# Kernel optimization log

Hardware: AMD Instinct MI355X
Metric: run time of the kernel (lower is better)

Reference implementation:

```python
import jax, jax.numpy as jnp
import numpy as np

B, N1, N2, D, K, KC = 2, 4096, 4096, 64, 16, 8
MLP = [128, 128, 128]
HID = [8, 8]


def _knn_idx(q, db, k):
    # q:[B,S,C] db:[B,M,C] -> indices of k smallest squared distances [B,S,k]
    d = (jnp.sum(q * q, -1)[..., None]
         - 2.0 * jnp.einsum('bsc,bmc->bsm', q, db)
         + jnp.sum(db * db, -1)[:, None, :])
    d = jnp.maximum(d, 0.0)
    _, idx = jax.lax.top_k(-d, k)
    return idx


def _group(points, idx):
    # points:[B,M,C], idx:[B,S,K] -> [B,S,K,C]
    return jax.vmap(lambda p, i: p[i])(points, idx)


def _conv_chain(x, params, act):
    # 1x1 Conv2d chain on x:[B,C,K,N]
    for w, b in params:
        x = act(jnp.einsum('oi,bikn->bokn', w, x) + b[None, :, None, None])
    return x


def setup_inputs():
    key = jax.random.key(0)
    ks = jax.random.split(key, 40)

    def p(i, shape, s=0.05):
        return jax.random.normal(ks[i], shape, jnp.float32) * s

    inp = {
        'xyz1': p(0, (B, 3, N1), 1.0), 'xyz2': p(1, (B, 3, N2), 1.0),
        'points1': p(2, (B, D, N1), 1.0), 'points2': p(3, (B, D, N2), 1.0),
        'vel1': p(4, (B, N1), 1.0), 'vel2': p(5, (B, N2), 1.0),
        'mask1': jnp.ones((B, N1), bool), 'mask2': jnp.ones((B, N2), bool),
        'final_cluster_coords': p(6, (B, N1, KC, 3), 1.0),
        'final_cluster_vel': p(7, (B, N1, KC), 1.0),
        'w_xyz': jnp.asarray(0.4, jnp.float32),
        'w_vel': jnp.asarray(0.2, jnp.float32),
        'w_points': jnp.asarray(0.4, jnp.float32),
    }
    dims = [2 * D + 3] + MLP
    for i in range(3):
        inp[f'mlp_w{i}'] = p(8 + i, (dims[i + 1], dims[i]))
        inp[f'mlp_b{i}'] = p(11 + i, (dims[i + 1],))
    wdims = [3] + HID + [MLP[-1]]
    for i in range(3):
        inp[f'wn1_w{i}'] = p(14 + i, (wdims[i + 1], wdims[i]), 0.5)
        inp[f'wn1_b{i}'] = p(17 + i, (wdims[i + 1],), 0.5)
        inp[f'wn2_w{i}'] = p(20 + i, (wdims[i + 1], wdims[i]), 0.5)
        inp[f'wn2_b{i}'] = p(23 + i, (wdims[i + 1],), 0.5)
    return inp


def reference(xyz1, xyz2, points1, points2, vel1, vel2, mask1, mask2,
              final_cluster_coords, final_cluster_vel,
              w_xyz, w_vel, w_points,
              mlp_w0, mlp_b0, mlp_w1, mlp_b1, mlp_w2, mlp_b2,
              wn1_w0, wn1_b0, wn1_w1, wn1_b1, wn1_w2, wn1_b2,
              wn2_w0, wn2_b0, wn2_w1, wn2_b1, wn2_w2, wn2_b2):
    leaky = lambda x: jnp.where(x >= 0, x, 0.1 * x)  # LeakyReLU(0.1)
    relu = jax.nn.relu
    x1 = xyz1.transpose(0, 2, 1)   # [B,N1,3]
    x2 = xyz2.transpose(0, 2, 1)   # [B,N2,3]
    p1 = points1.transpose(0, 2, 1)  # [B,N1,D]
    p2 = points2.transpose(0, 2, 1)  # [B,N2,D]

    u = final_cluster_coords / jnp.linalg.norm(final_cluster_coords, axis=-1, keepdims=True)
    ATA = jnp.einsum('bnki,bnkj->bnij', u, u) + 1e-6 * jnp.eye(3, dtype=u.dtype)
    ATb = jnp.einsum('bnki,bnk->bni', u, final_cluster_vel)
    v_world = jnp.linalg.solve(ATA, ATb[..., None])[..., 0]  # [B,N1,3]
    u1 = x1 / jnp.linalg.norm(x1, axis=-1, keepdims=True)
    err = jnp.abs(jnp.sum(v_world * u1, -1) - vel1)
    mask = err <= 5.0  # [B,N1]

    # --- cross-frame KNN in weighted feature space ---
    f1 = jnp.concatenate([w_xyz * x1, w_points * p1], -1)
    f2 = jnp.concatenate([w_xyz * x2, w_points * p2], -1)
    idx = _knn_idx(f1, f2, K)                       # [B,N1,K]
    dxyz = _group(x2, idx) - x1[:, :, None, :]      # [B,N1,K,3]
    gp2 = _group(p2, idx)                           # [B,N1,K,D]
    gp1 = jnp.broadcast_to(p1[:, :, None, :], gp2.shape)
    new_pts = jnp.concatenate([gp1, gp2, dxyz], -1).transpose(0, 3, 2, 1)  # [B,2D+3,K,N1]
    new_pts = _conv_chain(new_pts, [(mlp_w0, mlp_b0), (mlp_w1, mlp_b1), (mlp_w2, mlp_b2)], leaky)
    w1 = _conv_chain(dxyz.transpose(0, 3, 2, 1),
                     [(wn1_w0, wn1_b0), (wn1_w1, wn1_b1), (wn1_w2, wn1_b2)], relu)
    p2p = jnp.sum(w1 * new_pts, axis=2)  # [B,Cout,N1]

    # --- patch-to-patch aggregation with rigidity-weighted features ---
    mf = mask[..., None].astype(x1.dtype)
    w_r = mf * 0.9 + (1.0 - mf) * 0.1
    w_f = mf * 0.1 + (1.0 - mf) * 0.9
    comb = jnp.concatenate([w_f * f1, w_r * v_world], -1)
    idx2 = _knn_idx(comb, comb, K)
    dxyz2 = _group(x1, idx2) - x1[:, :, None, :]
    w2 = _conv_chain(dxyz2.transpose(0, 3, 2, 1),
                     [(wn2_w0, wn2_b0), (wn2_w1, wn2_b1), (wn2_w2, wn2_b2)], relu)
    gcost = _group(p2p.transpose(0, 2, 1), idx2)     # [B,N1,K,Cout]
    patch = jnp.sum(w2 * gcost.transpose(0, 3, 2, 1), axis=2)  # [B,Cout,N1]
    return patch, v_world
```

## Files before the change

kernel.cpp:

```cpp
#include <hip/hip_runtime.h>
#include <hip/hip_bf16.h>

typedef __hip_bfloat16 bf16;
typedef unsigned long long u64;
typedef __bf16 bf16x8 __attribute__((ext_vector_type(8)));
typedef __bf16 bf16x4 __attribute__((ext_vector_type(4)));
typedef _Float16 f16x8 __attribute__((ext_vector_type(8)));
typedef _Float16 f16x4 __attribute__((ext_vector_type(4)));
typedef float  f32x4  __attribute__((ext_vector_type(4)));

#define Bsz 2
#define Np  4096
#define Dch 64
#define Kn  16
#define KCn 8
#define DIMA 67
#define DIMB 70
#define CH  128
#define POSB 64
#define XS   168
#define TS   104
#define MS   24
#define MR   10
#define WNSZ 1256
#define PHALF (Bsz*Np*2*MS)


#define OFF_P1T  0
#define OFF_P2T  (Bsz*Np*Dch)
#define OFF_P2P  (2*Bsz*Np*Dch)
#define OFF_IDX1 (OFF_P2P + Bsz*Np*CH)
#define OFF_IDX2 (OFF_IDX1 + Bsz*Np*Kn)
#define OFF_F1N  (OFF_IDX2 + Bsz*Np*Kn)
#define OFF_F2N  (OFF_F1N + Bsz*Np)
#define OFF_CBN  (OFF_F2N + Bsz*Np)
#define OFF_WF   (OFF_CBN + Bsz*Np)
#define OFF_WR   (OFF_WF + Bsz*Np)
#define OFF_VW   (OFF_WR + Bsz*Np)
#define OFF_BF   (OFF_VW + 3*Bsz*Np)
#define BFSZ     (Bsz*Np*TS)
#define OFF_WPK  (OFF_BF + 3*BFSZ)

__device__ __forceinline__ int sniff_bf(const void* wxyz) {
    float v = __bfloat162float(((const bf16*)wxyz)[0]);
    return (fabsf(v - 0.4f) < 0.05f) ? 1 : 0;
}
__device__ __forceinline__ float ldin(const void* p, long i, int isbf) {
    return isbf ? __bfloat162float(((const bf16*)p)[i]) : ((const float*)p)[i];
}
__device__ __forceinline__ void stout(void* p, long i, float v, int isbf) {
    if (isbf) ((bf16*)p)[i] = __float2bfloat16(v);
    else      ((float*)p)[i] = v;
}
__device__ __forceinline__ u64 shfl_xor_u64(u64 v, int m) {
    int lo = __shfl_xor((int)(unsigned)(v & 0xFFFFFFFFu), m, 64);
    int hi = __shfl_xor((int)(unsigned)(v >> 32), m, 64);
    return ((u64)(unsigned)hi << 32) | (unsigned)lo;
}
__device__ __forceinline__ void hlsplit(float x, _Float16* hp, _Float16* lp) {
    _Float16 h = (_Float16)x;
    *hp = h;
    *lp = (_Float16)(x - (float)h);
}
__device__ __forceinline__ void gload_lds16(const void* g, void* l) {
    __builtin_amdgcn_global_load_lds(
        (const __attribute__((address_space(1))) unsigned int*)g,
        (__attribute__((address_space(3))) unsigned int*)l,
        16, 0, 0);
}

__global__ __launch_bounds__(256) void pack_kernel(
    const void* __restrict__ wxyz,
    const void* __restrict__ mw0, const void* __restrict__ mb0,
    const void* __restrict__ mw1, const void* __restrict__ mb1,
    const void* __restrict__ mw2, const void* __restrict__ mb2,
    const void* __restrict__ n1w0, const void* __restrict__ n1b0,
    const void* __restrict__ n1w1, const void* __restrict__ n1b1,
    const void* __restrict__ n1w2, const void* __restrict__ n1b2,
    const void* __restrict__ n2w0, const void* __restrict__ n2b0,
    const void* __restrict__ n2w1, const void* __restrict__ n2b1,
    const void* __restrict__ n2w2, const void* __restrict__ n2b2,
    __bf16* __restrict__ Wp, float* __restrict__ bp,
    float* __restrict__ wn1p, float* __restrict__ wn2p)
{
    int isbf = sniff_bf(wxyz);
    int t0 = blockIdx.x * 256 + threadIdx.x;
    int NT = gridDim.x * 256;
    for (int i = t0; i < 3*CH*XS; i += NT) {
        int L = i / (CH*XS), r = i - L*(CH*XS);
        int o = r / XS, c = r - o*XS;
        int dimIn = (L == 0) ? 131 : 128;
        const void* Wg = (L == 0) ? mw0 : ((L == 1) ? mw1 : mw2);
        Wp[i] = (c < dimIn) ? (__bf16)ldin(Wg, (long)o*dimIn + c, isbf) : (__bf16)0.f;
    }
    for (int i = t0; i < 3*CH; i += NT) {
        int L = i >> 7, o = i & 127;
        const void* Bg = (L == 0) ? mb0 : ((L == 1) ? mb1 : mb2);
        bp[i] = ldin(Bg, o, isbf);
    }
    for (int i = t0; i < WNSZ; i += NT) {
        float v1, v2;
        if (i < 1024)      { v1 = ldin(n1w2, i, isbf);        v2 = ldin(n2w2, i, isbf); }
        else if (i < 1152) { v1 = ldin(n1b2, i-1024, isbf);   v2 = ldin(n2b2, i-1024, isbf); }
        else if (i < 1176) { v1 = ldin(n1w0, i-1152, isbf);   v2 = ldin(n2w0, i-1152, isbf); }
        else if (i < 1184) { v1 = ldin(n1b0, i-1176, isbf);   v2 = ldin(n2b0, i-1176, isbf); }
        else if (i < 1248) { v1 = ldin(n1w1, i-1184, isbf);   v2 = ldin(n2w1, i-1184, isbf); }
        else               { v1 = ldin(n1b1, i-1248, isbf);   v2 = ldin(n2b1, i-1248, isbf); }
        wn1p[i] = v1; wn2p[i] = v2;
    }
}

__global__ __launch_bounds__(64) void prep_pt_kernel(
    const void* __restrict__ xyz1, const void* __restrict__ vel1,
    const void* __restrict__ fcc, const void* __restrict__ fcv,
    const void* __restrict__ wxyz, const void* __restrict__ xyz2,
    _Float16* __restrict__ f1hi, _Float16* __restrict__ f1lo,
    _Float16* __restrict__ cbhi, _Float16* __restrict__ cblo,
    float* __restrict__ f1n, float* __restrict__ cbn,
    float* __restrict__ wfA, float* __restrict__ wrA, float* __restrict__ vwA,
    void* __restrict__ outv,
    _Float16* __restrict__ f2hi, float* __restrict__ f2n)
{
    int isbf = sniff_bf(wxyz);
    float wx = ldin(wxyz, 0, isbf);
    if (blockIdx.x >= (Bsz*Np)/64) {
        int gid = (blockIdx.x - (Bsz*Np)/64) * 64 + threadIdx.x;
        int b = gid >> 12, n = gid & (Np - 1);
        _Float16* fh = f2hi + (size_t)gid * TS;
        float nn = 0.f;
        #pragma unroll
        for (int j = 0; j < 3; j++) {
            float v = wx * ldin(xyz2, (b*3+j)*Np + n, isbf);
            nn += v*v;
            fh[64+j] = (_Float16)v;
        }
        f2n[gid] = nn;
        return;
    }
    int gid = blockIdx.x * 64 + threadIdx.x;
    int b = gid >> 12, n = gid & (Np - 1);

    float a00=0.f,a01=0.f,a02=0.f,a11=0.f,a12=0.f,a22=0.f,r0=0.f,r1=0.f,r2=0.f;
    for (int k = 0; k < KCn; k++) {
        long base = ((long)gid * KCn + k) * 3;
        float x = ldin(fcc, base, isbf), y = ldin(fcc, base+1, isbf), z = ldin(fcc, base+2, isbf);
        float inv = 1.0f / sqrtf(x*x + y*y + z*z);
        float ux = x*inv, uy = y*inv, uz = z*inv;
        a00 += ux*ux; a01 += ux*uy; a02 += ux*uz;
        a11 += uy*uy; a12 += uy*uz; a22 += uz*uz;
        float v = ldin(fcv, (long)gid * KCn + k, isbf);
        r0 += ux*v; r1 += uy*v; r2 += uz*v;
    }
    a00 += 1e-6f; a11 += 1e-6f; a22 += 1e-6f;
    float c00 = a11*a22 - a12*a12;
    float c01 = a02*a12 - a01*a22;
    float c02 = a01*a12 - a02*a11;
    float det = a00*c00 + a01*c01 + a02*c02;
    float id  = 1.0f / det;
    float c11 = a00*a22 - a02*a02;
    float c12 = a01*a02 - a00*a12;
    float c22 = a00*a11 - a01*a01;
    float vx = (c00*r0 + c01*r1 + c02*r2) * id;
    float vy = (c01*r0 + c11*r1 + c12*r2) * id;
    float vz = (c02*r0 + c12*r1 + c22*r2) * id;

    stout(outv, (long)Bsz*CH*Np + gid*3 + 0, vx, isbf);
    stout(outv, (long)Bsz*CH*Np + gid*3 + 1, vy, isbf);
    stout(outv, (long)Bsz*CH*Np + gid*3 + 2, vz, isbf);
    vwA[gid*3+0] = vx; vwA[gid*3+1] = vy; vwA[gid*3+2] = vz;

    float x0 = ldin(xyz1, (b*3+0)*Np + n, isbf);
    float x1 = ldin(xyz1, (b*3+1)*Np + n, isbf);
    float x2 = ldin(xyz1, (b*3+2)*Np + n, isbf);
    float invn = 1.0f / sqrtf(x0*x0 + x1*x1 + x2*x2);
    float dotv = vx*(x0*invn) + vy*(x1*invn) + vz*(x2*invn);
    float err = fabsf(dotv - ldin(vel1, gid, isbf));
    bool msk = (err <= 5.0f);
    float w_f = msk ? 0.1f : 0.9f;
    float w_r = msk ? 0.9f : 0.1f;
    wfA[gid] = w_f; wrA[gid] = w_r;

    _Float16* fh = f1hi + (size_t)gid * TS;
    _Float16* fl = f1lo + (size_t)gid * TS;
    _Float16* ch = cbhi + (size_t)gid * TS;
    _Float16* cl = cblo + (size_t)gid * TS;
    float nn = 0.f, cn = 0.f;
    float xs[3] = {x0, x1, x2};
    #pragma unroll
    for (int j = 0; j < 3; j++) {
        float v = wx * xs[j]; nn += v*v; hlsplit(v, fh+64+j, fl+64+j);
        float c = w_f * v;    cn += c*c; hlsplit(c, ch+64+j, cl+64+j);
    }
    float vv[3] = {vx, vy, vz};
    #pragma unroll
    for (int j = 0; j < 3; j++) {
        float c = w_r * vv[j]; cn += c*c; hlsplit(c, ch+67+j, cl+67+j);
    }
    f1n[gid] = nn;
    cbn[gid] = cn;
}

__global__ __launch_bounds__(256) void prep_ch_kernel(
    const void* __restrict__ points1, const void* __restrict__ points2,
    const void* __restrict__ wxyz, const void* __restrict__ wpts,
    const float* __restrict__ wfA,
    _Float16* __restrict__ f1hi, _Float16* __restrict__ f1lo,
    _Float16* __restrict__ cbhi, _Float16* __restrict__ cblo,
    float* __restrict__ p1t, float* __restrict__ f1n, float* __restrict__ cbn,
    _Float16* __restrict__ f2hi,
    float* __restrict__ p2t, float* __restrict__ f2n)
{
    __shared__ float tile[16 * 64];
    int t = threadIdx.x;
    int isbf = sniff_bf(wxyz);
    float wp = ldin(wpts, 0, isbf);
    int fr = blockIdx.x >> 9;
    int g0 = (blockIdx.x & 511) * 16;
    int b = g0 >> 12;
    const void* pts = fr ? points2 : points1;
    _Float16* fhi = fr ? f2hi : f1hi;
    float* ptt = fr ? p2t : p1t;
    float* fn  = fr ? f2n : f1n;
    int do_cb = !fr;

    {
        int n16 = t & 15, cc = t >> 4;
        int n = (g0 + n16) & (Np - 1);
        #pragma unroll
        for (int it = 0; it < 4; it++) {
            int c = cc + it * 16;
            tile[n16 * 64 + c] = ldin(pts, (long)(b * Dch + c) * Np + n, isbf);
        }
    }
    __syncthreads();

    int p = t >> 4, j = t & 15;
    int gid = g0 + p;
    float wf = do_cb ? wfA[gid] : 0.f;
    float nn = 0.f, cn = 0.f;
    f16x4 h4, l4, ch4, cl4;
    float pv4[4];
    #pragma unroll
    for (int i = 0; i < 4; i++) {
        float pv = tile[p * 64 + 4 * j + i];
        pv4[i] = pv;
        float v = wp * pv; nn += v * v;
        _Float16 hh, ll; hlsplit(v, &hh, &ll);
        h4[i] = hh; l4[i] = ll;
        float c = wf * v; cn += c * c;
        _Float16 chh, cll; hlsplit(c, &chh, &cll);
        ch4[i] = chh; cl4[i] = cll;
    }
    *(f16x4*)(fhi + (size_t)gid * TS + 4 * j) = h4;
    if (do_cb) {
        *(f16x4*)(f1lo + (size_t)gid * TS + 4 * j) = l4;
        *(f16x4*)(cbhi + (size_t)gid * TS + 4 * j) = ch4;
        *(f16x4*)(cblo + (size_t)gid * TS + 4 * j) = cl4;
    }
    float4 pq = { pv4[0], pv4[1], pv4[2], pv4[3] };
    *(float4*)(ptt + (size_t)gid * Dch + 4 * j) = pq;

    #pragma unroll
    for (int s = 1; s < 16; s <<= 1) {
        nn += __shfl_xor(nn, s, 64);
        cn += __shfl_xor(cn, s, 64);
    }
    if (j == 0) {
        fn[gid] += nn;
        if (do_cb) cbn[gid] += cn;
    }
}

__global__ __launch_bounds__(256, 8) void knn_kernel(
    const _Float16* __restrict__ f1hi, const _Float16* __restrict__ f1lo,
    const float* __restrict__ f1n,
    const _Float16* __restrict__ f2hi, const float* __restrict__ f2n,
    const _Float16* __restrict__ cbhi, const _Float16* __restrict__ cblo,
    const float* __restrict__ cbn,
    unsigned* __restrict__ part)
{
    __shared__ __align__(16) _Float16 Th[64 * TS];
    __shared__ unsigned dkey[64 * 17 + 16];

    int t = threadIdx.x;
    int prob = blockIdx.x >> 10;
    int bid = blockIdx.x & 1023;
    int qblk = bid >> 1, half = bid & 1;
    int qbase = qblk * 16;
    int b = qbase >> 12;

    const _Float16* qhi = prob ? cbhi : f1hi;
    const _Float16* qlo = prob ? cblo : f1lo;
    const float*  qn  = prob ? cbn  : f1n;
    const _Float16* dbh = (prob ? cbhi : f2hi) + (size_t)b * Np * TS;
    const float*  dnb = (prob ? cbn  : f2n) + (size_t)b * Np;
    unsigned* pout = part + (size_t)prob * PHALF;

    int qi = t >> 4, w = t & 15;
    int wv = t >> 6, lane = t & 63, quad = lane >> 4, col = lane & 15;

    f16x8 qfh[3], qfl[3];
    #pragma unroll
    for (int kb = 0; kb < 3; kb++) {
        qfh[kb] = *(const f16x8*)(qhi + (size_t)(qbase + col) * TS + kb*32 + quad*8);
        qfl[kb] = *(const f16x8*)(qlo + (size_t)(qbase + col) * TS + kb*32 + quad*8);
    }
    float qn4[4];
    #pragma unroll
    for (int r = 0; r < 4; r++) qn4[r] = qn[qbase + quad*4 + r];

    unsigned bd[MR];
    #pragma unroll
    for (int i = 0; i < MR; i++) bd[i] = 0xFFFFFFFFu;

    for (int T = 0; T < Np / 128; T++) {
        int Tg = half * (Np / 128) + T;
        {
            const float4* sh = (const float4*)(dbh + (size_t)Tg * 64 * TS);
            float4* dh = (float4*)Th;
            for (int i = t; i < 64 * 13; i += 256)
                gload_lds16(sh + i, dh + i);
        }
        __syncthreads();

        f32x4 acc = {0.f, 0.f, 0.f, 0.f};
        #pragma unroll
        for (int kb = 0; kb < 3; kb++) {
            f16x8 bh = *(const f16x8*)(Th + (wv*16 + col) * TS + kb*32 + quad*8);
            acc = __builtin_amdgcn_mfma_f32_16x16x32_f16(qfh[kb], bh, acc, 0, 0, 0);
            acc = __builtin_amdgcn_mfma_f32_16x16x32_f16(qfl[kb], bh, acc, 0, 0, 0);
        }
        float tn = dnb[Tg * 64 + wv*16 + col];
        unsigned lidx = (unsigned)(T*64 + wv*16 + col);
        #pragma unroll
        for (int r = 0; r < 4; r++) {
            int m = quad*4 + r;
            float d = fmaxf(qn4[r] - 2.f * acc[r] + tn, 0.f);
            dkey[(wv*16 + col) * 17 + m] = (__float_as_uint(d) & 0xFFFFF800u) | lidx;
        }
        __syncthreads();

        #pragma unroll
        for (int p = 0; p < 4; p++) {
            unsigned key = dkey[(w + p*16) * 17 + qi];
            if (key < bd[MR-1]) {
                bd[MR-1] = key;
                #pragma unroll
                for (int j = MR-2; j >= 0; j--) {
                    unsigned lo = bd[j] < bd[j+1] ? bd[j] : bd[j+1];
                    unsigned hi = bd[j] < bd[j+1] ? bd[j+1] : bd[j];
                    bd[j] = lo; bd[j+1] = hi;
                }
            }
        }
    }

    unsigned win1 = 0, win2 = 0;
    #pragma unroll
    for (int o = 0; o < MS; o++) {
        unsigned v = bd[0];
        #pragma unroll
        for (int s = 1; s < 16; s <<= 1) {
            unsigned u = (unsigned)__shfl_xor((int)v, s, 64);
            v = u < v ? u : v;
        }
        if (w == o) win1 = v;
        if (w == o - 16) win2 = v;
        if (bd[0] == v) {
            #pragma unroll
            for (int j = 0; j < MR-1; j++) bd[j] = bd[j+1];
            bd[MR-1] = 0xFFFFFFFFu;
        }
    }
    size_t base = ((size_t)(qbase + qi) * 2 + half) * MS;
    pout[base + w] = (win1 & 0x7FFu) + (unsigned)half * 2048u;
    if (w < MS - 16) pout[base + 16 + w] = (win2 & 0x7FFu) + (unsigned)half * 2048u;
}

__global__ __launch_bounds__(256) void knn_rescue_kernel(
    const unsigned* __restrict__ part,
    const void* __restrict__ xyz1, const void* __restrict__ xyz2,
    const float* __restrict__ p1t, const float* __restrict__ p2t,
    const float* __restrict__ f1n, const float* __restrict__ f2n,
    const float* __restrict__ cbn,
    const float* __restrict__ wfA, const float* __restrict__ wrA,
    const float* __restrict__ vwA,
    const void* __restrict__ wxyz, const void* __restrict__ wpts,
    int* __restrict__ idx1, int* __restrict__ idx2)
{
    __shared__ float qrow[4][64];
    __shared__ float qmisc[4][12];

    int t = threadIdx.x, wv = t >> 6, l = t & 63;
    int isbf = sniff_bf(wxyz);
    float wx = ldin(wxyz, 0, isbf), wp = ldin(wpts, 0, isbf);
    int mode = blockIdx.x >> 11;
    int qb = blockIdx.x & 2047;
    int q = qb * 4 + wv;
    int b = q >> 12, n = q & (Np - 1);

    const void* xyzc = mode ? xyz1 : xyz2;
    const float* ptc = mode ? p1t : p2t;
    const float* qnA = mode ? cbn : f1n;
    const float* cnA = mode ? cbn : f2n;
    const unsigned* pp = part + (size_t)mode * PHALF;
    int* out = mode ? idx2 : idx1;

    if (l < 16) ((float4*)qrow[wv])[l] = *(const float4*)(p1t + (size_t)q * Dch + l*4);
    if (l == 16) {
        qmisc[wv][0] = ldin(xyz1, (b*3+0)*Np + n, isbf);
        qmisc[wv][1] = ldin(xyz1, (b*3+1)*Np + n, isbf);
        qmisc[wv][2] = ldin(xyz1, (b*3+2)*Np + n, isbf);
        qmisc[wv][3] = qnA[q];
        if (mode == 1) {
            qmisc[wv][4] = wfA[q]; qmisc[wv][5] = wrA[q];
            qmisc[wv][6] = vwA[q*3+0]; qmisc[wv][7] = vwA[q*3+1]; qmisc[wv][8] = vwA[q*3+2];
        }
    }
    __syncthreads();

    u64 key = 0xFFFFFFFFFFFFFFFFULL;
    if (l < 2 * MS) {
        unsigned pk = pp[(size_t)q * (2*MS) + l];
        int m = (int)pk & (Np - 1);
        const float* crow = ptc + (size_t)(b * Np + m) * Dch;
        float sp = 0.f;
        #pragma unroll
        for (int i = 0; i < 16; i++) {
            float4 qv = ((const float4*)qrow[wv])[i];
            float4 cv = *(const float4*)(crow + i*4);
            sp = fmaf(qv.x, cv.x, sp); sp = fmaf(qv.y, cv.y, sp);
            sp = fmaf(qv.z, cv.z, sp); sp = fmaf(qv.w, cv.w, sp);
        }
        float sx = 0.f;
        #pragma unroll
        for (int j = 0; j < 3; j++)
            sx = fmaf(qmisc[wv][j], ldin(xyzc, (b*3+j)*Np + m, isbf), sx);
        float dot;
        if (mode == 0) {
            dot = wx*wx*sx + wp*wp*sp;
        } else {
            float sv = qmisc[wv][6]*vwA[(size_t)(b*Np+m)*3+0]
                     + qmisc[wv][7]*vwA[(size_t)(b*Np+m)*3+1]
                     + qmisc[wv][8]*vwA[(size_t)(b*Np+m)*3+2];
            dot = qmisc[wv][4]*wfA[b*Np+m]*(wx*wx*sx + wp*wp*sp)
                + qmisc[wv][5]*wrA[b*Np+m]*sv;
        }
        float d = fmaxf(qmisc[wv][3] - 2.f*dot + cnA[b*Np + m], 0.f);
        key = ((u64)__float_as_uint(d) << 32) | (unsigned)m;
    }

    #pragma unroll
    for (int k = 2; k <= 64; k <<= 1) {
        #pragma unroll
        for (int j = k >> 1; j >= 1; j >>= 1) {
            u64 p = shfl_xor_u64(key, j);
            bool up   = ((l & k) == 0);
            bool lowh = ((l & j) == 0);
            u64 mn = (key < p) ? key : p;
            u64 mx = (key < p) ? p : key;
            key = (up == lowh) ? mn : mx;
        }
    }
    if (l < Kn) out[(size_t)q * Kn + l] = (int)(key & 0xFFFFFFFFu);
}

__global__ __launch_bounds__(256) void mlp_mfma_kernel(
    const void* __restrict__ xyz1, const void* __restrict__ xyz2,
    const float* __restrict__ p1t, const float* __restrict__ p2t,
    const int* __restrict__ idx1, const void* __restrict__ wxyz,
    const __bf16* __restrict__ Wp, const float* __restrict__ bp,
    const float* __restrict__ wn1p,
    float* __restrict__ p2p)
{
    __shared__ __align__(16) __bf16 X[POSB * XS];
    __shared__ __align__(16) __bf16 Wt[CH * XS];
    __shared__ float biasS[CH];
    __shared__ float dxs[POSB * 4];
    __shared__ float h2s[POSB * 8];
    __shared__ float wnS[WNSZ];
    __shared__ int   nidx[POSB];

    int t = threadIdx.x;
    int isbf = sniff_bf(wxyz);
    int ng0 = blockIdx.x * 4;
    int bidx = ng0 >> 12;

    for (int i = t; i < WNSZ; i += 256) wnS[i] = wn1p[i];
    if (t < POSB) {
        int nl = t >> 4, k = t & 15;
        nidx[t] = idx1[(size_t)(ng0 + nl) * Kn + k] & (Np - 1);
    }
    __syncthreads();

    for (int i = t; i < POSB * 32; i += 256) {
        int pos = i >> 5, g = i & 31;
        int nl = pos >> 4, ng = ng0 + nl, m = nidx[pos];
        float4 v = (g < 16) ? ((const float4*)(p1t + (size_t)ng * Dch))[g]
                            : ((const float4*)(p2t + (size_t)(bidx*Np + m) * Dch))[g - 16];
        bf16x4 o4 = { (__bf16)v.x, (__bf16)v.y, (__bf16)v.z, (__bf16)v.w };
        *(bf16x4*)(X + pos * XS + g * 4) = o4;
    }
    if (t < POSB) {
        int nl = t >> 4, ng = ng0 + nl, m = nidx[t];
        #pragma unroll
        for (int j = 0; j < 3; j++) {
            float dv = ldin(xyz2, (bidx*3+j)*Np + m, isbf)
                     - ldin(xyz1, (bidx*3+j)*Np + (ng & (Np-1)), isbf);
            X[t*XS + 128 + j] = (__bf16)dv;
            dxs[t*4 + j] = dv;
        }
        for (int c = 131; c < XS; c++) X[t*XS + c] = (__bf16)0.f;
    }

    int wv = t >> 6, lane = t & 63, quad = lane >> 4, col = lane & 15;

    #pragma unroll
    for (int L = 0; L < 3; L++) {
        const int KK = (L == 0) ? 160 : 128;
        __syncthreads();
        {
            const float4* src = (const float4*)(Wp + (size_t)L * CH * XS);
            for (int i = t; i < CH * XS / 8; i += 256) ((float4*)Wt)[i] = src[i];
        }
        if (t < CH) biasS[t] = bp[L * CH + t];
        __syncthreads();

        f32x4 acc[8];
        #pragma unroll
        for (int nt = 0; nt < 8; nt++) {
            float bv = biasS[nt * 16 + col];
            f32x4 a; a[0] = bv; a[1] = bv; a[2] = bv; a[3] = bv;
            acc[nt] = a;
        }
        for (int kb = 0; kb < KK / 32; kb++) {
            bf16x8 af = *(const bf16x8*)(X + (16*wv + col) * XS + kb*32 + quad*8);
            #pragma unroll
            for (int nt = 0; nt < 8; nt++) {
                bf16x8 bfr = *(const bf16x8*)(Wt + (nt*16 + col) * XS + kb*32 + quad*8);
                acc[nt] = __builtin_amdgcn_mfma_f32_16x16x32_bf16(af, bfr, acc[nt], 0, 0, 0);
            }
        }
        #pragma unroll
        for (int nt = 0; nt < 8; nt++) {
            #pragma unroll
            for (int r = 0; r < 4; r++) {
                float v = acc[nt][r];
                v = (v >= 0.f) ? v : 0.1f * v;
                X[(16*wv + quad*4 + r) * XS + nt*16 + col] = (__bf16)v;
            }
        }
    }
    __syncthreads();

    const float* wn_w2 = wnS;
    const float* wn_b2 = wnS + 1024;
    const float* wn_w0 = wnS + 1152;
    const float* wn_b0 = wnS + 1176;
    const float* wn_w1 = wnS + 1184;
    const float* wn_b1 = wnS + 1248;

    if (t < POSB) {
        float h1[8];
        #pragma unroll
        for (int j = 0; j < 8; j++) {
            float s = wn_b0[j];
            #pragma unroll
            for (int i = 0; i < 3; i++) s += wn_w0[j*3+i] * dxs[t*4+i];
            h1[j] = fmaxf(s, 0.f);
        }
        #pragma unroll
        for (int j = 0; j < 8; j++) {
            float s = wn_b1[j];
            #pragma unroll
            for (int i = 0; i < 8; i++) s += wn_w1[j*8+i] * h1[i];
            h2s[t*8+j] = fmaxf(s, 0.f);
        }
    }
    __syncthreads();

    for (int o = t; o < 4 * CH; o += 256) {
        int nl = o >> 7, c = o & 127;
        float acc = 0.f;
        for (int k = 0; k < Kn; k++) {
            int pos = nl*16 + k;
            float s = wn_b2[c];
            #pragma unroll
            for (int j = 0; j < 8; j++) s += wn_w2[c*8+j] * h2s[pos*8+j];
            s = fmaxf(s, 0.f);
            acc += s * (float)X[pos * XS + c];
        }
        p2p[(size_t)(ng0 + nl) * CH + c] = acc;
    }
}

__global__ __launch_bounds__(256) void patch_kernel(
    const void* __restrict__ xyz1, const float* __restrict__ p2p,
    const int* __restrict__ idx2, const void* __restrict__ wxyz,
    const float* __restrict__ wn2p,
    void* __restrict__ outp)
{
    __shared__ float wnS[WNSZ];
    __shared__ float h2s[128 * 8];
    __shared__ int   nid[128];
    __shared__ float outS[8][132];

    int t = threadIdx.x;
    int bn0 = blockIdx.x * 8;
    int isbf = sniff_bf(wxyz);
    int b = bn0 >> 12, n0 = bn0 & (Np - 1);

    for (int i = t; i < WNSZ; i += 256) wnS[i] = wn2p[i];
    if (t < 128) nid[t] = idx2[(size_t)bn0 * Kn + t] & (Np - 1);
    __syncthreads();

    const float* w2s = wnS;
    const float* b2s = wnS + 1024;
    const float* w0s = wnS + 1152;
    const float* b0s = wnS + 1176;
    const float* w1s = wnS + 1184;
    const float* b1s = wnS + 1248;

    if (t < 128) {
        int q = t >> 4;
        int n = n0 + q;
        int m = nid[t];
        float dx[3];
        #pragma unroll
        for (int j = 0; j < 3; j++)
            dx[j] = ldin(xyz1, (b*3+j)*Np + m, isbf) - ldin(xyz1, (b*3+j)*Np + n, isbf);
        float h1[8];
        #pragma unroll
        for (int j = 0; j < 8; j++) {
            float s = b0s[j];
            #pragma unroll
            for (int i = 0; i < 3; i++) s += w0s[j*3+i] * dx[i];
            h1[j] = fmaxf(s, 0.f);
        }
        #pragma unroll
        for (int j = 0; j < 8; j++) {
            float s = b1s[j];
            #pragma unroll
            for (int i = 0; i < 8; i++) s += w1s[j*8+i] * h1[i];
            h2s[t*8+j] = fmaxf(s, 0.f);
        }
    }
    __syncthreads();

    {
        int c = t & 127, qh = t >> 7;
        #pragma unroll
        for (int qq = 0; qq < 4; qq++) {
            int q = qh + qq*2;
            float acc = 0.f;
            for (int k = 0; k < Kn; k++) {
                int mm = nid[q*16 + k];
                float s = b2s[c];
                #pragma unroll
                for (int j = 0; j < 8; j++) s += w2s[c*8+j] * h2s[(q*16+k)*8+j];
                s = fmaxf(s, 0.f);
                acc += s * p2p[(size_t)(b * Np + mm) * CH + c];
            }
            outS[q][c] = acc;
        }
    }
    __syncthreads();

    if (t < 128) {
        int c = t;
        size_t obase = (size_t)(b*CH + c) * Np + n0;
        if (isbf) {
            bf16x8 o;
            #pragma unroll
            for (int i = 0; i < 8; i++) o[i] = (__bf16)outS[i][c];
            *(bf16x8*)((__bf16*)outp + obase) = o;
        } else {
            float4 o1 = { outS[0][c], outS[1][c], outS[2][c], outS[3][c] };
            float4 o2 = { outS[4][c], outS[5][c], outS[6][c], outS[7][c] };
            *(float4*)((float*)outp + obase) = o1;
            *(float4*)((float*)outp + obase + 4) = o2;
        }
    }
}

extern "C" void kernel_launch(void* const* d_in, const int* in_sizes, int n_in,
                              void* d_out, int out_size, void* d_ws, size_t ws_size,
                              hipStream_t stream)
{
    const void* xyz1    = d_in[0];
    const void* xyz2    = d_in[1];
    const void* points1 = d_in[2];
    const void* points2 = d_in[3];
    const void* vel1    = d_in[4];
    const void* fcc     = d_in[8];
    const void* fcv     = d_in[9];
    const void* wxyz    = d_in[10];
    const void* wpts    = d_in[12];
    const void* mw0 = d_in[13]; const void* mb0 = d_in[14];
    const void* mw1 = d_in[15]; const void* mb1 = d_in[16];
    const void* mw2 = d_in[17]; const void* mb2 = d_in[18];
    const void* w1w0 = d_in[19]; const void* w1b0 = d_in[20];
    const void* w2w0 = d_in[21]; const void* w2b0 = d_in[22];
    const void* w1w1 = d_in[23]; const void* w1b1 = d_in[24];
    const void* w2w1 = d_in[25]; const void* w2b1 = d_in[26];
    const void* w1w2 = d_in[27]; const void* w1b2 = d_in[28];
    const void* w2w2 = d_in[29]; const void* w2b2 = d_in[30];

    float* ws = (float*)d_ws;
    float* p1t  = ws + OFF_P1T;
    float* p2t  = ws + OFF_P2T;
    float* p2p  = ws + OFF_P2P;
    int* idx1 = (int*)(ws + OFF_IDX1);
    int* idx2 = (int*)(ws + OFF_IDX2);
    float* f1n = ws + OFF_F1N;
    float* f2n = ws + OFF_F2N;
    float* cbn = ws + OFF_CBN;
    float* wfA = ws + OFF_WF;
    float* wrA = ws + OFF_WR;
    float* vwA = ws + OFF_VW;
    _Float16* f1hi = (_Float16*)(ws + OFF_BF);
    _Float16* f1lo = f1hi + BFSZ;
    _Float16* f2hi = f1lo + BFSZ;
    _Float16* f2lo = f2hi + BFSZ;
    _Float16* cbhi = f2lo + BFSZ;
    _Float16* cblo = cbhi + BFSZ;
    __bf16* Wp  = (__bf16*)(ws + OFF_WPK);
    float*  bp  = ws + OFF_WPK + (3*CH*XS)/2;
    float*  wn1p = bp + 3*CH;
    float*  wn2p = wn1p + WNSZ;
    unsigned* part = (unsigned*)(ws + OFF_P2P);

    hipMemsetAsync(f1hi, 0, (size_t)6 * BFSZ * sizeof(_Float16), stream);

    pack_kernel<<<64, 256, 0, stream>>>(wxyz,
        mw0, mb0, mw1, mb1, mw2, mb2,
        w1w0, w1b0, w1w1, w1b1, w1w2, w1b2,
        w2w0, w2b0, w2w1, w2b1, w2w2, w2b2,
        Wp, bp, wn1p, wn2p);
    prep_pt_kernel<<<2*(Bsz*Np)/64, 64, 0, stream>>>(xyz1, vel1, fcc, fcv, wxyz, xyz2,
        f1hi, f1lo, cbhi, cblo, f1n, cbn, wfA, wrA, vwA, d_out, f2hi, f2n);
    prep_ch_kernel<<<2*(Bsz*Np)/16, 256, 0, stream>>>(points1, points2, wxyz, wpts, wfA,
        f1hi, f1lo, cbhi, cblo, p1t, f1n, cbn, f2hi, p2t, f2n);
    knn_kernel<<<2*(Bsz*Np)/16*2, 256, 0, stream>>>(f1hi, f1lo, f1n, f2hi, f2n,
        cbhi, cblo, cbn, part);
    knn_rescue_kernel<<<2*(Bsz*Np)/4, 256, 0, stream>>>(part, xyz1, xyz2, p1t, p2t,
        f1n, f2n, cbn, wfA, wrA, vwA, wxyz, wpts, idx1, idx2);
    mlp_mfma_kernel<<<(Bsz*Np)/4, 256, 0, stream>>>(xyz1, xyz2, p1t, p2t, idx1, wxyz,
        Wp, bp, wn1p, p2p);
    patch_kernel<<<(Bsz*Np)/8, 256, 0, stream>>>(xyz1, p2p, idx2, wxyz, wn2p, d_out);
}
```

Before: 365.6 us.

## Drop fp16 low-part split in KNN, shrink candidate list, fuse setup kernels

The KNN distance GEMM now uses only the fp16 high part of each feature, which halves the MFMA count and drops the lo-buffer reads and writes. The per-query candidate list shrinks from 10 to 8 entries. The pack and per-point prep kernels are merged into one launch, and the big memset is replaced by zeroing only the padding lanes. Candidate selection becomes less precise, so the rescue pass has to absorb more near-ties, and neighbours could be missed if fp16 error exceeds the margin the rescue covers.

```diff
diff --git a/kernel.cpp b/kernel.cpp
--- a/kernel.cpp
+++ b/kernel.cpp
@@ -21,7 +21,7 @@
 #define XS   168
 #define TS   104
 #define MS   24
-#define MR   10
+#define MR   8
 #define WNSZ 1256
 #define PHALF (Bsz*Np*2*MS)
 
@@ -57,11 +57,6 @@
     int hi = __shfl_xor((int)(unsigned)(v >> 32), m, 64);
     return ((u64)(unsigned)hi << 32) | (unsigned)lo;
 }
-__device__ __forceinline__ void hlsplit(float x, _Float16* hp, _Float16* lp) {
-    _Float16 h = (_Float16)x;
-    *hp = h;
-    *lp = (_Float16)(x - (float)h);
-}
 __device__ __forceinline__ void gload_lds16(const void* g, void* l) {
     __builtin_amdgcn_global_load_lds(
         (const __attribute__((address_space(1))) unsigned int*)g,
@@ -69,8 +64,15 @@
         16, 0, 0);
 }
 
-__global__ __launch_bounds__(256) void pack_kernel(
-    const void* __restrict__ wxyz,
+__global__ __launch_bounds__(256) void setup_kernel(
+    const void* __restrict__ xyz1, const void* __restrict__ vel1,
+    const void* __restrict__ fcc, const void* __restrict__ fcv,
+    const void* __restrict__ wxyz, const void* __restrict__ xyz2,
+    _Float16* __restrict__ f1hi, _Float16* __restrict__ cbhi,
+    float* __restrict__ f1n, float* __restrict__ cbn,
+    float* __restrict__ wfA, float* __restrict__ wrA, float* __restrict__ vwA,
+    void* __restrict__ outv,
+    _Float16* __restrict__ f2hi, float* __restrict__ f2n,
     const void* __restrict__ mw0, const void* __restrict__ mb0,
     const void* __restrict__ mw1, const void* __restrict__ mb1,
     const void* __restrict__ mw2, const void* __restrict__ mb2,
@@ -83,50 +85,46 @@
     __bf16* __restrict__ Wp, float* __restrict__ bp,
     float* __restrict__ wn1p, float* __restrict__ wn2p)
 {
+    int bid = blockIdx.x, t = threadIdx.x;
     int isbf = sniff_bf(wxyz);
-    int t0 = blockIdx.x * 256 + threadIdx.x;
-    int NT = gridDim.x * 256;
-    for (int i = t0; i < 3*CH*XS; i += NT) {
-        int L = i / (CH*XS), r = i - L*(CH*XS);
-        int o = r / XS, c = r - o*XS;
-        int dimIn = (L == 0) ? 131 : 128;
-        const void* Wg = (L == 0) ? mw0 : ((L == 1) ? mw1 : mw2);
-        Wp[i] = (c < dimIn) ? (__bf16)ldin(Wg, (long)o*dimIn + c, isbf) : (__bf16)0.f;
-    }
-    for (int i = t0; i < 3*CH; i += NT) {
-        int L = i >> 7, o = i & 127;
-        const void* Bg = (L == 0) ? mb0 : ((L == 1) ? mb1 : mb2);
-        bp[i] = ldin(Bg, o, isbf);
-    }
-    for (int i = t0; i < WNSZ; i += NT) {
-        float v1, v2;
-        if (i < 1024)      { v1 = ldin(n1w2, i, isbf);        v2 = ldin(n2w2, i, isbf); }
-        else if (i < 1152) { v1 = ldin(n1b2, i-1024, isbf);   v2 = ldin(n2b2, i-1024, isbf); }
-        else if (i < 1176) { v1 = ldin(n1w0, i-1152, isbf);   v2 = ldin(n2w0, i-1152, isbf); }
-        else if (i < 1184) { v1 = ldin(n1b0, i-1176, isbf);   v2 = ldin(n2b0, i-1176, isbf); }
-        else if (i < 1248) { v1 = ldin(n1w1, i-1184, isbf);   v2 = ldin(n2w1, i-1184, isbf); }
-        else               { v1 = ldin(n1b1, i-1248, isbf);   v2 = ldin(n2b1, i-1248, isbf); }
-        wn1p[i] = v1; wn2p[i] = v2;
-    }
-}
-
-__global__ __launch_bounds__(64) void prep_pt_kernel(
-    const void* __restrict__ xyz1, const void* __restrict__ vel1,
-    const void* __restrict__ fcc, const void* __restrict__ fcv,
-    const void* __restrict__ wxyz, const void* __restrict__ xyz2,
-    _Float16* __restrict__ f1hi, _Float16* __restrict__ f1lo,
-    _Float16* __restrict__ cbhi, _Float16* __restrict__ cblo,
-    float* __restrict__ f1n, float* __restrict__ cbn,
-    float* __restrict__ wfA, float* __restrict__ wrA, float* __restrict__ vwA,
-    void* __restrict__ outv,
-    _Float16* __restrict__ f2hi, float* __restrict__ f2n)
-{
-    int isbf = sniff_bf(wxyz);
+    const f16x8 z8 = {0,0,0,0,0,0,0,0};
+
+    if (bid >= 64) {
+        int t0 = (bid - 64) * 256 + t;
+        int NT = 64 * 256;
+        for (int i = t0; i < 3*CH*XS; i += NT) {
+            int L = i / (CH*XS), r = i - L*(CH*XS);
+            int o = r / XS, c = r - o*XS;
+            int dimIn = (L == 0) ? 131 : 128;
+            const void* Wg = (L == 0) ? mw0 : ((L == 1) ? mw1 : mw2);
+            Wp[i] = (c < dimIn) ? (__bf16)ldin(Wg, (long)o*dimIn + c, isbf) : (__bf16)0.f;
+        }
+        for (int i = t0; i < 3*CH; i += NT) {
+            int L = i >> 7, o = i & 127;
+            const void* Bg = (L == 0) ? mb0 : ((L == 1) ? mb1 : mb2);
+            bp[i] = ldin(Bg, o, isbf);
+        }
+        for (int i = t0; i < WNSZ; i += NT) {
+            float v1, v2;
+            if (i < 1024)      { v1 = ldin(n1w2, i, isbf);        v2 = ldin(n2w2, i, isbf); }
+            else if (i < 1152) { v1 = ldin(n1b2, i-1024, isbf);   v2 = ldin(n2b2, i-1024, isbf); }
+            else if (i < 1176) { v1 = ldin(n1w0, i-1152, isbf);   v2 = ldin(n2w0, i-1152, isbf); }
+            else if (i < 1184) { v1 = ldin(n1b0, i-1176, isbf);   v2 = ldin(n2b0, i-1176, isbf); }
+            else if (i < 1248) { v1 = ldin(n1w1, i-1184, isbf);   v2 = ldin(n2w1, i-1184, isbf); }
+            else               { v1 = ldin(n1b1, i-1248, isbf);   v2 = ldin(n2b1, i-1248, isbf); }
+            wn1p[i] = v1; wn2p[i] = v2;
+        }
+        return;
+    }
+
     float wx = ldin(wxyz, 0, isbf);
-    if (blockIdx.x >= (Bsz*Np)/64) {
-        int gid = (blockIdx.x - (Bsz*Np)/64) * 64 + threadIdx.x;
+
+    if (bid >= 32) {
+        int gid = (bid - 32) * 256 + t;
         int b = gid >> 12, n = gid & (Np - 1);
         _Float16* fh = f2hi + (size_t)gid * TS;
+        #pragma unroll
+        for (int i = 64; i < TS; i += 8) *(f16x8*)(fh + i) = z8;
         float nn = 0.f;
         #pragma unroll
         for (int j = 0; j < 3; j++) {
@@ -137,7 +135,8 @@
         f2n[gid] = nn;
         return;
     }
-    int gid = blockIdx.x * 64 + threadIdx.x;
+
+    int gid = bid * 256 + t;
     int b = gid >> 12, n = gid & (Np - 1);
 
     float a00=0.f,a01=0.f,a02=0.f,a11=0.f,a12=0.f,a22=0.f,r0=0.f,r1=0.f,r2=0.f;
@@ -181,20 +180,20 @@
     wfA[gid] = w_f; wrA[gid] = w_r;
 
     _Float16* fh = f1hi + (size_t)gid * TS;
-    _Float16* fl = f1lo + (size_t)gid * TS;
     _Float16* ch = cbhi + (size_t)gid * TS;
-    _Float16* cl = cblo + (size_t)gid * TS;
+    #pragma unroll
+    for (int i = 64; i < TS; i += 8) { *(f16x8*)(fh + i) = z8; *(f16x8*)(ch + i) = z8; }
     float nn = 0.f, cn = 0.f;
     float xs[3] = {x0, x1, x2};
     #pragma unroll
     for (int j = 0; j < 3; j++) {
-        float v = wx * xs[j]; nn += v*v; hlsplit(v, fh+64+j, fl+64+j);
-        float c = w_f * v;    cn += c*c; hlsplit(c, ch+64+j, cl+64+j);
+        float v = wx * xs[j]; nn += v*v; fh[64+j] = (_Float16)v;
+        float c = w_f * v;    cn += c*c; ch[64+j] = (_Float16)c;
     }
     float vv[3] = {vx, vy, vz};
     #pragma unroll
     for (int j = 0; j < 3; j++) {
-        float c = w_r * vv[j]; cn += c*c; hlsplit(c, ch+67+j, cl+67+j);
+        float c = w_r * vv[j]; cn += c*c; ch[67+j] = (_Float16)c;
     }
     f1n[gid] = nn;
     cbn[gid] = cn;
@@ -204,8 +203,7 @@
     const void* __restrict__ points1, const void* __restrict__ points2,
     const void* __restrict__ wxyz, const void* __restrict__ wpts,
     const float* __restrict__ wfA,
-    _Float16* __restrict__ f1hi, _Float16* __restrict__ f1lo,
-    _Float16* __restrict__ cbhi, _Float16* __restrict__ cblo,
+    _Float16* __restrict__ f1hi, _Float16* __restrict__ cbhi,
     float* __restrict__ p1t, float* __restrict__ f1n, float* __restrict__ cbn,
     _Float16* __restrict__ f2hi,
     float* __restrict__ p2t, float* __restrict__ f2n)
@@ -238,25 +236,19 @@
     int gid = g0 + p;
     float wf = do_cb ? wfA[gid] : 0.f;
     float nn = 0.f, cn = 0.f;
-    f16x4 h4, l4, ch4, cl4;
+    f16x4 h4, ch4;
     float pv4[4];
     #pragma unroll
     for (int i = 0; i < 4; i++) {
         float pv = tile[p * 64 + 4 * j + i];
         pv4[i] = pv;
         float v = wp * pv; nn += v * v;
-        _Float16 hh, ll; hlsplit(v, &hh, &ll);
-        h4[i] = hh; l4[i] = ll;
+        h4[i] = (_Float16)v;
         float c = wf * v; cn += c * c;
-        _Float16 chh, cll; hlsplit(c, &chh, &cll);
-        ch4[i] = chh; cl4[i] = cll;
+        ch4[i] = (_Float16)c;
     }
     *(f16x4*)(fhi + (size_t)gid * TS + 4 * j) = h4;
-    if (do_cb) {
-        *(f16x4*)(f1lo + (size_t)gid * TS + 4 * j) = l4;
-        *(f16x4*)(cbhi + (size_t)gid * TS + 4 * j) = ch4;
-        *(f16x4*)(cblo + (size_t)gid * TS + 4 * j) = cl4;
-    }
+    if (do_cb) *(f16x4*)(cbhi + (size_t)gid * TS + 4 * j) = ch4;
     float4 pq = { pv4[0], pv4[1], pv4[2], pv4[3] };
     *(float4*)(ptt + (size_t)gid * Dch + 4 * j) = pq;
 
@@ -272,11 +264,9 @@
 }
 
 __global__ __launch_bounds__(256, 8) void knn_kernel(
-    const _Float16* __restrict__ f1hi, const _Float16* __restrict__ f1lo,
-    const float* __restrict__ f1n,
+    const _Float16* __restrict__ f1hi, const float* __restrict__ f1n,
     const _Float16* __restrict__ f2hi, const float* __restrict__ f2n,
-    const _Float16* __restrict__ cbhi, const _Float16* __restrict__ cblo,
-    const float* __restrict__ cbn,
+    const _Float16* __restrict__ cbhi, const float* __restrict__ cbn,
     unsigned* __restrict__ part)
 {
     __shared__ __align__(16) _Float16 Th[64 * TS];
@@ -290,7 +280,6 @@
     int b = qbase >> 12;
 
     const _Float16* qhi = prob ? cbhi : f1hi;
-    const _Float16* qlo = prob ? cblo : f1lo;
     const float*  qn  = prob ? cbn  : f1n;
     const _Float16* dbh = (prob ? cbhi : f2hi) + (size_t)b * Np * TS;
     const float*  dnb = (prob ? cbn  : f2n) + (size_t)b * Np;
@@ -299,12 +288,10 @@
     int qi = t >> 4, w = t & 15;
     int wv = t >> 6, lane = t & 63, quad = lane >> 4, col = lane & 15;
 
-    f16x8 qfh[3], qfl[3];
-    #pragma unroll
-    for (int kb = 0; kb < 3; kb++) {
+    f16x8 qfh[3];
+    #pragma unroll
+    for (int kb = 0; kb < 3; kb++)
         qfh[kb] = *(const f16x8*)(qhi + (size_t)(qbase + col) * TS + kb*32 + quad*8);
-        qfl[kb] = *(const f16x8*)(qlo + (size_t)(qbase + col) * TS + kb*32 + quad*8);
-    }
     float qn4[4];
     #pragma unroll
     for (int r = 0; r < 4; r++) qn4[r] = qn[qbase + quad*4 + r];
@@ -328,7 +315,6 @@
         for (int kb = 0; kb < 3; kb++) {
             f16x8 bh = *(const f16x8*)(Th + (wv*16 + col) * TS + kb*32 + quad*8);
             acc = __builtin_amdgcn_mfma_f32_16x16x32_f16(qfh[kb], bh, acc, 0, 0, 0);
-            acc = __builtin_amdgcn_mfma_f32_16x16x32_f16(qfl[kb], bh, acc, 0, 0, 0);
         }
         float tn = dnb[Tg * 64 + wv*16 + col];
         unsigned lidx = (unsigned)(T*64 + wv*16 + col);
@@ -723,26 +709,22 @@
     _Float16* f2hi = f1lo + BFSZ;
     _Float16* f2lo = f2hi + BFSZ;
     _Float16* cbhi = f2lo + BFSZ;
-    _Float16* cblo = cbhi + BFSZ;
     __bf16* Wp  = (__bf16*)(ws + OFF_WPK);
     float*  bp  = ws + OFF_WPK + (3*CH*XS)/2;
     float*  wn1p = bp + 3*CH;
     float*  wn2p = wn1p + WNSZ;
     unsigned* part = (unsigned*)(ws + OFF_P2P);
 
-    hipMemsetAsync(f1hi, 0, (size_t)6 * BFSZ * sizeof(_Float16), stream);
-
-    pack_kernel<<<64, 256, 0, stream>>>(wxyz,
+    setup_kernel<<<128, 256, 0, stream>>>(xyz1, vel1, fcc, fcv, wxyz, xyz2,
+        f1hi, cbhi, f1n, cbn, wfA, wrA, vwA, d_out, f2hi, f2n,
         mw0, mb0, mw1, mb1, mw2, mb2,
         w1w0, w1b0, w1w1, w1b1, w1w2, w1b2,
         w2w0, w2b0, w2w1, w2b1, w2w2, w2b2,
         Wp, bp, wn1p, wn2p);
-    prep_pt_kernel<<<2*(Bsz*Np)/64, 64, 0, stream>>>(xyz1, vel1, fcc, fcv, wxyz, xyz2,
-        f1hi, f1lo, cbhi, cblo, f1n, cbn, wfA, wrA, vwA, d_out, f2hi, f2n);
     prep_ch_kernel<<<2*(Bsz*Np)/16, 256, 0, stream>>>(points1, points2, wxyz, wpts, wfA,
-        f1hi, f1lo, cbhi, cblo, p1t, f1n, cbn, f2hi, p2t, f2n);
-    knn_kernel<<<2*(Bsz*Np)/16*2, 256, 0, stream>>>(f1hi, f1lo, f1n, f2hi, f2n,
-        cbhi, cblo, cbn, part);
+        f1hi, cbhi, p1t, f1n, cbn, f2hi, p2t, f2n);
+    knn_kernel<<<2*(Bsz*Np)/16*2, 256, 0, stream>>>(f1hi, f1n, f2hi, f2n,
+        cbhi, cbn, part);
     knn_rescue_kernel<<<2*(Bsz*Np)/4, 256, 0, stream>>>(part, xyz1, xyz2, p1t, p2t,
         f1n, f2n, cbn, wfA, wrA, vwA, wxyz, wpts, idx1, idx2);
     mlp_mfma_kernel<<<(Bsz*Np)/4, 256, 0, stream>>>(xyz1, xyz2, p1t, p2t, idx1, wxyz,
```

After: 352.6 us. 1.04x faster.
